# Performance work log

Measured on AMD Instinct MI355X. Metric: run time of the kernel, lower is better.

The kernel has to match this reference:

```python
import jax, jax.numpy as jnp
import numpy as np

K_MASK = -2.3819763e38  # gemma masking constant


def apply_rope(inputs, positions, head_dim):
    # inputs: [B, T, N, H], positions: [B, T]
    half = head_dim // 2
    fraction = 2.0 * jnp.arange(half, dtype=jnp.float32) / head_dim
    timescale = 10000.0 ** fraction                      # [half]
    sinusoid = positions[..., None].astype(jnp.float32) / timescale  # [B, T, half]
    sin = jnp.sin(sinusoid)[:, :, None, :]               # [B, T, 1, half]
    cos = jnp.cos(sinusoid)[:, :, None, :]
    first, second = jnp.split(inputs, 2, axis=-1)
    out = jnp.concatenate([first * cos - second * sin,
                           second * cos + first * sin], axis=-1)
    return out.astype(inputs.dtype)


def setup_inputs() -> dict:
    key = jax.random.key(0)
    k0, k1, k2, k3 = jax.random.split(key, 4)
    B, T, D, N, H = 4, 1024, 2048, 16, 128
    x = jax.random.normal(k0, (B, T, D), dtype=jnp.float32)
    wq = jax.random.normal(k1, (N, D, H), dtype=jnp.float32) * 0.02
    wkv = jax.random.normal(k2, (2, 1, D, H), dtype=jnp.float32) * 0.02  # MQA: 1 kv head
    wo = jax.random.normal(k3, (N, H, D), dtype=jnp.float32) * 0.02
    segment_pos = jnp.broadcast_to(jnp.arange(T, dtype=jnp.int32), (B, T))
    attn_mask = jnp.broadcast_to(jnp.tril(jnp.ones((T, T), dtype=bool)), (B, T, T))
    return {"x": x, "wq": wq, "wkv": wkv, "wo": wo,
            "segment_pos": segment_pos, "attn_mask": attn_mask}


def reference(x, wq, wkv, wo, segment_pos, attn_mask):
    N, _, H = wq.shape
    # projections
    q = jnp.einsum('BTD,NDH->BTNH', x, wq)          # [B,T,N,H]
    kv = jnp.einsum('BSD,CKDH->CBSKH', x, wkv)      # [2,B,S,1,H]
    k, v = kv[0], kv[1]
    # RoPE + scaling
    q = apply_rope(q, segment_pos, H) * (H ** -0.5)
    k = apply_rope(k, segment_pos, H)
    # MQA head repeat: 1 kv head -> N heads
    k = jnp.repeat(k, N, axis=-2)                   # [B,S,N,H]
    v = jnp.repeat(v, N, axis=-2)
    # attention with manual masked softmax
    logits = jnp.einsum('BTNH,BSNH->BTNS', q, k)
    padded = jnp.where(attn_mask[:, :, None, :], logits, K_MASK)
    probs = jax.nn.softmax(padded, axis=-1).astype(k.dtype)
    encoded = jnp.einsum('BTNS,BSNH->BTNH', probs, v)
    return jnp.einsum('BTNH,NHD->BTD', encoded, wo)
```

## Files before the change

### kernel.cpp

```cpp
#include <hip/hip_runtime.h>
#include <cstdint>
#include <cstddef>

typedef unsigned short u16;
typedef __attribute__((ext_vector_type(8))) short bf16x8;
typedef __attribute__((ext_vector_type(4))) float f32x4;
typedef __attribute__((ext_vector_type(16))) float f32x16;
typedef __attribute__((ext_vector_type(4))) uint32_t u32x4;

#define B_ 4
#define T_ 1024
#define D_ 2048
#define N_ 16
#define H_ 128
#define BT_ (B_ * T_)
#define KMASK (-2.3819763e38f)

__device__ __forceinline__ u16 f2bf(float f) {
  uint32_t u = __builtin_bit_cast(uint32_t, f);
  u += 0x7FFFu + ((u >> 16) & 1u);
  return (u16)(u >> 16);
}
__device__ __forceinline__ float bf2f(uint32_t u) {
  return __builtin_bit_cast(float, u << 16);
}

__device__ __forceinline__ float xhalf_max(float x) {
  return fmaxf(x, __shfl_xor(x, 32, 64));
}
__device__ __forceinline__ float xhalf_add(float x) {
  return x + __shfl_xor(x, 32, 64);
}

__device__ __forceinline__ void gload16(const void* g, void* l) {
  __builtin_amdgcn_global_load_lds((const __attribute__((address_space(1))) void*)g,
                                   (__attribute__((address_space(3))) void*)l, 16, 0, 0);
}

__global__ __launch_bounds__(256) void convert_x_kernel(const float* __restrict__ x,
                                                        u16* __restrict__ xb) {
  int i = (blockIdx.x * 256 + threadIdx.x) * 8;
  float4 v0 = *(const float4*)(x + i);
  float4 v1 = *(const float4*)(x + i + 4);
  uint4 o;
  o.x = (uint32_t)f2bf(v0.x) | ((uint32_t)f2bf(v0.y) << 16);
  o.y = (uint32_t)f2bf(v0.z) | ((uint32_t)f2bf(v0.w) << 16);
  o.z = (uint32_t)f2bf(v1.x) | ((uint32_t)f2bf(v1.y) << 16);
  o.w = (uint32_t)f2bf(v1.z) | ((uint32_t)f2bf(v1.w) << 16);
  *(uint4*)(xb + i) = o;
}

__global__ __launch_bounds__(256) void transpose_kernel(const float* __restrict__ src,
                                                        u16* __restrict__ dst, int R, int C) {
  __shared__ float tile[32][33];
  const int z = blockIdx.z;
  const float* s = src + (size_t)z * R * C;
  u16* d = dst + (size_t)z * R * C;
  const int tx = threadIdx.x, ty = threadIdx.y;
  const int r0 = blockIdx.y * 32, c0 = blockIdx.x * 32;
#pragma unroll
  for (int i = 0; i < 4; ++i)
    tile[ty + i * 8][tx] = s[(size_t)(r0 + ty + i * 8) * C + (c0 + tx)];
  __syncthreads();
#pragma unroll
  for (int i = 0; i < 4; ++i)
    d[(size_t)(c0 + ty + i * 8) * R + (r0 + tx)] = f2bf(tile[tx][ty + i * 8]);
}

__global__ __launch_bounds__(256) void rope_table_kernel(float* __restrict__ costab,
                                                         float* __restrict__ sintab) {
  int idx = blockIdx.x * 256 + threadIdx.x;
  int p = idx >> 6, i = idx & 63;
  float ts = powf(10000.0f, (float)i * (1.0f / 64.0f));
  float ang = (float)p / ts;
  costab[idx] = cosf(ang);
  sintab[idx] = sinf(ang);
}

__global__ __launch_bounds__(256) void proj_gemm_kernel(
    const u16* __restrict__ xb, const u16* __restrict__ wqT, const u16* __restrict__ wkvT,
    u16* __restrict__ qraw, u16* __restrict__ kraw, u16* __restrict__ vT) {
  __shared__ alignas(16) u16 a_lds[128 * 64];
  __shared__ alignas(16) u16 b_lds[128 * 64];
  const int bid = blockIdx.x;
  const int newbid = (bid & 7) * 72 + (bid >> 3);
  const int y = newbid >> 5;
  const int m0 = (newbid & 31) * 128;
  const u16* Bt = (y < N_) ? (wqT + (size_t)y * H_ * D_) : (wkvT + (size_t)(y - N_) * H_ * D_);
  const int tid = threadIdx.x;
  const int w = tid >> 6, lane = tid & 63;
  const int g = lane >> 4, li = lane & 15;
  const int mrow = (w >> 1) * 64, wc = (w & 1) * 64;
  f32x4 acc[4][4];
#pragma unroll
  for (int i = 0; i < 4; ++i)
#pragma unroll
    for (int j = 0; j < 4; ++j) acc[i][j] = (f32x4){0.f, 0.f, 0.f, 0.f};

  for (int k0 = 0; k0 < D_; k0 += 64) {
    __syncthreads();
#pragma unroll
    for (int it = 0; it < 4; ++it) {
      int chunk = it * 256 + tid;
      int row = chunk >> 3, cu = chunk & 7;
      gload16(xb + (size_t)(m0 + row) * D_ + k0 + ((cu ^ (row & 7)) << 3), &a_lds[chunk * 8]);
    }
#pragma unroll
    for (int it = 0; it < 4; ++it) {
      int chunk = it * 256 + tid;
      int row = chunk >> 3, cu = chunk & 7;
      gload16(Bt + (size_t)row * D_ + k0 + ((cu ^ (row & 7)) << 3), &b_lds[chunk * 8]);
    }
    __syncthreads();
#pragma unroll
    for (int c2 = 0; c2 < 2; ++c2) {
      bf16x8 af[4], bfr[4];
#pragma unroll
      for (int i = 0; i < 4; ++i) {
        int row = mrow + i * 16 + li;
        af[i] = *(const bf16x8*)((const char*)a_lds +
                                 row * 128 + ((c2 * 64 + g * 16) ^ ((row & 7) << 4)));
      }
#pragma unroll
      for (int j = 0; j < 4; ++j) {
        int row = wc + j * 16 + li;
        bfr[j] = *(const bf16x8*)((const char*)b_lds +
                                  row * 128 + ((c2 * 64 + g * 16) ^ ((row & 7) << 4)));
      }
#pragma unroll
      for (int i = 0; i < 4; ++i)
#pragma unroll
        for (int j = 0; j < 4; ++j)
          acc[i][j] = __builtin_amdgcn_mfma_f32_16x16x32_bf16(af[i], bfr[j], acc[i][j], 0, 0, 0);
    }
  }

  const int b = m0 >> 10;
  if (y == N_ + 1) {
    const int tbase0 = (m0 & 1023) + mrow;
#pragma unroll
    for (int i = 0; i < 4; ++i) {
      int tbase = tbase0 + i * 16 + g * 4;
#pragma unroll
      for (int j = 0; j < 4; ++j) {
        int h = wc + j * 16 + li;
        ushort4 pk;
        pk.x = f2bf(acc[i][j][0]);
        pk.y = f2bf(acc[i][j][1]);
        pk.z = f2bf(acc[i][j][2]);
        pk.w = f2bf(acc[i][j][3]);
        *(ushort4*)(vT + ((size_t)(b * H_ + h)) * T_ + tbase) = pk;
      }
    }
  } else {
    size_t rowbase = (y < N_) ? ((size_t)(b * N_ + y) * T_ + (m0 & 1023)) : (size_t)m0;
    u16* dst0 = (y < N_) ? qraw : kraw;
#pragma unroll
    for (int i = 0; i < 4; ++i)
#pragma unroll
      for (int r = 0; r < 4; ++r) {
        int trow = mrow + i * 16 + g * 4 + r;
        u16* dst = dst0 + (rowbase + trow) * H_;
#pragma unroll
        for (int j = 0; j < 4; ++j) dst[wc + j * 16 + li] = f2bf(acc[i][j][r]);
      }
  }
}

__global__ __launch_bounds__(256) void rope_apply_k_kernel(
    const u16* __restrict__ kraw, const int* __restrict__ segment_pos,
    const float* __restrict__ costab, const float* __restrict__ sintab,
    u16* __restrict__ kb) {
  const int rid = blockIdx.x * 8 + (threadIdx.x >> 5);
  const int j = threadIdx.x & 31;
  const u16* src = kraw + (size_t)rid * H_;
  u16* dst = kb + (size_t)rid * H_;
  int p = segment_pos[rid];
  p = p < 0 ? 0 : (p > 1023 ? 1023 : p);
  uint32_t ua = *(const uint32_t*)(src + 2 * j);
  uint32_t ub = *(const uint32_t*)(src + 64 + 2 * j);
  float2 cv = *(const float2*)(costab + p * 64 + 2 * j);
  float2 sv = *(const float2*)(sintab + p * 64 + 2 * j);
  float f1a = bf2f(ua & 0xffffu), f1b = bf2f(ua >> 16);
  float f2a = bf2f(ub & 0xffffu), f2b = bf2f(ub >> 16);
  *(uint32_t*)(dst + 2 * j) =
      (uint32_t)f2bf(f1a * cv.x - f2a * sv.x) | ((uint32_t)f2bf(f1b * cv.y - f2b * sv.y) << 16);
  *(uint32_t*)(dst + 64 + 2 * j) =
      (uint32_t)f2bf(f2a * cv.x + f1a * sv.x) | ((uint32_t)f2bf(f2b * cv.y + f1b * sv.y) << 16);
}

__global__ __launch_bounds__(128) void attn_kernel(
    const u16* __restrict__ qraw, const u16* __restrict__ kb, const u16* __restrict__ vT,
    const int* __restrict__ segment_pos, const float* __restrict__ costab,
    const float* __restrict__ sintab, u16* __restrict__ enc) {
  __shared__ alignas(16) u16 k_lds[2][64 * 128];
  __shared__ alignas(16) u16 v_lds[128 * 64];
  const int bx = blockIdx.x;
  const int qt = 15 - (bx >> 6);
  const int bn = bx & 63;
  const int b = bn >> 4, n = bn & 15;
  const int tid = threadIdx.x, w = tid >> 6, lane = tid & 63;
  const int l31 = lane & 31, hi = lane >> 5;
  const int t = qt * 64 + w * 32 + l31;

  bf16x8 qf[8];
  {
    const u16* qrow = qraw + ((size_t)(b * N_ + n) * T_ + t) * H_;
#pragma unroll
    for (int kc = 0; kc < 8; ++kc) qf[kc] = *(const bf16x8*)(qrow + kc * 16 + hi * 8);
    int p = segment_pos[b * T_ + t];
    p = p < 0 ? 0 : (p > 1023 ? 1023 : p);
    const float scale = 0.12751743342f;
#pragma unroll
    for (int kc = 0; kc < 4; ++kc) {
      const float* cp = costab + p * 64 + kc * 16 + hi * 8;
      const float* sp = sintab + p * 64 + kc * 16 + hi * 8;
#pragma unroll
      for (int e = 0; e < 8; ++e) {
        float cv = cp[e], sv = sp[e];
        float f1 = bf2f((u16)qf[kc][e]);
        float f2 = bf2f((u16)qf[kc + 4][e]);
        qf[kc][e] = (short)f2bf((f1 * cv - f2 * sv) * scale);
        qf[kc + 4][e] = (short)f2bf((f2 * cv + f1 * sv) * scale);
      }
    }
  }

  f32x16 o[4];
#pragma unroll
  for (int hc = 0; hc < 4; ++hc)
#pragma unroll
    for (int r = 0; r < 16; ++r) o[hc][r] = 0.f;
  float m_ = -3e38f, lsum = 0.f;

  auto stageK = [&](int buf, int s0) {
#pragma unroll
    for (int it = 0; it < 8; ++it) {
      int chunk = it * 128 + tid;
      int row = chunk >> 4, cu = chunk & 15;
      gload16(kb + ((size_t)b * T_ + s0 + row) * H_ + ((cu ^ (row & 15)) << 3),
              &k_lds[buf][chunk * 8]);
    }
  };
  auto stageV = [&](int s0) {
#pragma unroll
    for (int it = 0; it < 8; ++it) {
      int chunk = it * 128 + tid;
      int row = chunk >> 3, cu = chunk & 7;
      gload16(vT + ((size_t)(b * H_ + row)) * T_ + s0 + ((cu ^ (row & 7)) << 3),
              &v_lds[chunk * 8]);
    }
  };

  const int nst = qt + 1;
  stageK(0, 0);
  int cur = 0;
  for (int st = 0; st < nst; ++st) {
    const int s0 = st * 64;
    const bool pre = (st + 1 < nst);
    stageV(s0);
    if (pre) stageK(cur ^ 1, s0 + 64);
    if (pre) asm volatile("s_waitcnt vmcnt(16)" ::: "memory");
    else     asm volatile("s_waitcnt vmcnt(8)" ::: "memory");
    __builtin_amdgcn_sched_barrier(0);
    __builtin_amdgcn_s_barrier();

    f32x16 sacc[2];
#pragma unroll
    for (int sub = 0; sub < 2; ++sub)
#pragma unroll
      for (int r = 0; r < 16; ++r) sacc[sub][r] = 0.f;
    __builtin_amdgcn_s_setprio(1);
#pragma unroll
    for (int kc = 0; kc < 8; ++kc)
#pragma unroll
      for (int sub = 0; sub < 2; ++sub) {
        int srow = sub * 32 + l31;
        bf16x8 kf = *(const bf16x8*)((const char*)&k_lds[cur][0] + srow * 256 +
                                     ((kc * 32 + hi * 16) ^ ((srow & 15) << 4)));
        sacc[sub] = __builtin_amdgcn_mfma_f32_32x32x16_bf16(kf, qf[kc], sacc[sub], 0, 0, 0);
      }
    __builtin_amdgcn_s_setprio(0);

    if (st == qt) {
#pragma unroll
      for (int sub = 0; sub < 2; ++sub)
#pragma unroll
        for (int r = 0; r < 16; ++r) {
          int s = s0 + sub * 32 + (r & 3) + 8 * (r >> 2) + 4 * hi;
          if (s > t) sacc[sub][r] = KMASK;
        }
    }

    float mx = -3e38f;
#pragma unroll
    for (int sub = 0; sub < 2; ++sub)
#pragma unroll
      for (int r = 0; r < 16; ++r) mx = fmaxf(mx, sacc[sub][r]);
    mx = xhalf_max(mx);
    if (__any(mx - m_ > 11.5f)) {
      float mn = fmaxf(m_, mx);
      float alpha = exp2f(m_ - mn);
      m_ = mn;
      lsum *= alpha;
#pragma unroll
      for (int hc = 0; hc < 4; ++hc)
#pragma unroll
        for (int r = 0; r < 16; ++r) o[hc][r] *= alpha;
    }
    float ps = 0.f;
#pragma unroll
    for (int sub = 0; sub < 2; ++sub)
#pragma unroll
      for (int r = 0; r < 16; ++r) {
        float pv = exp2f(sacc[sub][r] - m_);
        sacc[sub][r] = pv;
        ps += pv;
      }
    lsum += xhalf_add(ps);

    if (pre) asm volatile("s_waitcnt vmcnt(8)" ::: "memory");
    else     asm volatile("s_waitcnt vmcnt(0)" ::: "memory");
    __builtin_amdgcn_sched_barrier(0);
    __builtin_amdgcn_s_barrier();

    __builtin_amdgcn_s_setprio(1);
#pragma unroll
    for (int sc = 0; sc < 4; ++sc) {
      const int sub = sc >> 1, rb = (sc & 1) * 8;
      uint32_t a0, a1, b0, b1;
      asm("v_cvt_pk_bf16_f32 %0, %1, %2" : "=v"(a0) : "v"(sacc[sub][rb + 0]), "v"(sacc[sub][rb + 1]));
      asm("v_cvt_pk_bf16_f32 %0, %1, %2" : "=v"(a1) : "v"(sacc[sub][rb + 2]), "v"(sacc[sub][rb + 3]));
      asm("v_cvt_pk_bf16_f32 %0, %1, %2" : "=v"(b0) : "v"(sacc[sub][rb + 4]), "v"(sacc[sub][rb + 5]));
      asm("v_cvt_pk_bf16_f32 %0, %1, %2" : "=v"(b1) : "v"(sacc[sub][rb + 6]), "v"(sacc[sub][rb + 7]));
      uint32_t pa0 = (uint32_t)__shfl_xor((int)a0, 32, 64);
      uint32_t pa1 = (uint32_t)__shfl_xor((int)a1, 32, 64);
      uint32_t pb0 = (uint32_t)__shfl_xor((int)b0, 32, 64);
      uint32_t pb1 = (uint32_t)__shfl_xor((int)b1, 32, 64);
      uint32_t d0 = hi ? pb0 : a0;
      uint32_t d1 = hi ? pb1 : a1;
      uint32_t d2 = hi ? b0 : pa0;
      uint32_t d3 = hi ? b1 : pa1;
      u32x4 pdv = (u32x4){d0, d1, d2, d3};
      bf16x8 pf = __builtin_bit_cast(bf16x8, pdv);
#pragma unroll
      for (int hc = 0; hc < 4; ++hc) {
        int hrow = hc * 32 + l31;
        bf16x8 vf = *(const bf16x8*)((const char*)v_lds + hrow * 128 +
                                     ((sc * 32 + hi * 16) ^ ((hrow & 7) << 4)));
        o[hc] = __builtin_amdgcn_mfma_f32_32x32x16_bf16(vf, pf, o[hc], 0, 0, 0);
      }
    }
    __builtin_amdgcn_s_setprio(0);
    __builtin_amdgcn_s_barrier();
    cur ^= 1;
  }

  float inv = 1.0f / lsum;
  u16* dst = enc + ((size_t)(b * T_ + t)) * (N_ * H_) + n * H_;
#pragma unroll
  for (int hc = 0; hc < 4; ++hc)
#pragma unroll
    for (int rq = 0; rq < 4; ++rq) {
      ushort4 pk;
      pk.x = f2bf(o[hc][rq * 4 + 0] * inv);
      pk.y = f2bf(o[hc][rq * 4 + 1] * inv);
      pk.z = f2bf(o[hc][rq * 4 + 2] * inv);
      pk.w = f2bf(o[hc][rq * 4 + 3] * inv);
      *(ushort4*)(dst + hc * 32 + rq * 8 + hi * 4) = pk;
    }
}

__global__ __launch_bounds__(256) void out_gemm_kernel(const u16* __restrict__ enc,
                                                       const u16* __restrict__ woT,
                                                       float* __restrict__ out) {
  __shared__ alignas(16) u16 a_lds[128 * 64];
  __shared__ alignas(16) u16 b_lds[128 * 64];
  const int bid = blockIdx.x;
  const int newbid = (bid & 7) * 64 + (bid >> 3);
  const int m0 = (newbid & 31) * 128;
  const int n0 = (newbid >> 5) * 128;
  const int tid = threadIdx.x, w = tid >> 6, lane = tid & 63;
  const int g = lane >> 4, li = lane & 15;
  const int mrow = (w >> 1) * 64, wc = (w & 1) * 64;
  f32x4 acc[4][4];
#pragma unroll
  for (int i = 0; i < 4; ++i)
#pragma unroll
    for (int j = 0; j < 4; ++j) acc[i][j] = (f32x4){0.f, 0.f, 0.f, 0.f};

  for (int k0 = 0; k0 < D_; k0 += 64) {
    __syncthreads();
#pragma unroll
    for (int it = 0; it < 4; ++it) {
      int chunk = it * 256 + tid;
      int row = chunk >> 3, cu = chunk & 7;
      gload16(enc + (size_t)(m0 + row) * D_ + k0 + ((cu ^ (row & 7)) << 3), &a_lds[chunk * 8]);
    }
#pragma unroll
    for (int it = 0; it < 4; ++it) {
      int chunk = it * 256 + tid;
      int row = chunk >> 3, cu = chunk & 7;
      gload16(woT + (size_t)(n0 + row) * D_ + k0 + ((cu ^ (row & 7)) << 3), &b_lds[chunk * 8]);
    }
    __syncthreads();
#pragma unroll
    for (int c2 = 0; c2 < 2; ++c2) {
      bf16x8 af[4], bfr[4];
#pragma unroll
      for (int i = 0; i < 4; ++i) {
        int row = mrow + i * 16 + li;
        af[i] = *(const bf16x8*)((const char*)a_lds +
                                 row * 128 + ((c2 * 64 + g * 16) ^ ((row & 7) << 4)));
      }
#pragma unroll
      for (int j = 0; j < 4; ++j) {
        int row = wc + j * 16 + li;
        bfr[j] = *(const bf16x8*)((const char*)b_lds +
                                  row * 128 + ((c2 * 64 + g * 16) ^ ((row & 7) << 4)));
      }
#pragma unroll
      for (int i = 0; i < 4; ++i)
#pragma unroll
        for (int j = 0; j < 4; ++j)
          acc[i][j] = __builtin_amdgcn_mfma_f32_16x16x32_bf16(af[i], bfr[j], acc[i][j], 0, 0, 0);
    }
  }
#pragma unroll
  for (int i = 0; i < 4; ++i)
#pragma unroll
    for (int r = 0; r < 4; ++r) {
      int bt = m0 + mrow + i * 16 + g * 4 + r;
      float* dst = out + (size_t)bt * D_ + n0 + wc;
#pragma unroll
      for (int j = 0; j < 4; ++j) dst[j * 16 + li] = acc[i][j][r];
    }
}

extern "C" void kernel_launch(void* const* d_in, const int* in_sizes, int n_in,
                              void* d_out, int out_size, void* d_ws, size_t ws_size,
                              hipStream_t stream) {
  const float* x = (const float*)d_in[0];
  const float* wq = (const float*)d_in[1];
  const float* wkv = (const float*)d_in[2];
  const float* wo = (const float*)d_in[3];
  const int* segment_pos = (const int*)d_in[4];
  float* out = (float*)d_out;

  char* ws = (char*)d_ws;
  size_t off = 0;
  auto alloc = [&](size_t bytes) -> void* {
    void* p = ws + off;
    off += (bytes + 255) & ~(size_t)255;
    return p;
  };
  u16* xb   = (u16*)alloc((size_t)BT_ * D_ * 2);
  u16* wqT  = (u16*)alloc((size_t)N_ * H_ * D_ * 2);
  u16* wkvT = (u16*)alloc((size_t)2 * H_ * D_ * 2);
  u16* woT  = (u16*)alloc((size_t)D_ * N_ * H_ * 2);
  u16* qraw = (u16*)alloc((size_t)B_ * N_ * T_ * H_ * 2);
  u16* kb   = (u16*)alloc((size_t)B_ * T_ * H_ * 2);
  u16* kraw = (u16*)alloc((size_t)B_ * T_ * H_ * 2);
  u16* vT   = (u16*)alloc((size_t)B_ * H_ * T_ * 2);
  u16* enc  = (u16*)alloc((size_t)BT_ * N_ * H_ * 2);
  float* costab = (float*)alloc(1024 * 64 * 4);
  float* sintab = (float*)alloc(1024 * 64 * 4);

  convert_x_kernel<<<BT_ * D_ / 8 / 256, 256, 0, stream>>>(x, xb);
  dim3 tb(32, 8);
  transpose_kernel<<<dim3(H_ / 32, D_ / 32, N_), tb, 0, stream>>>(wq, wqT, D_, H_);
  transpose_kernel<<<dim3(H_ / 32, D_ / 32, 2), tb, 0, stream>>>(wkv, wkvT, D_, H_);
  transpose_kernel<<<dim3(D_ / 32, D_ / 32, 1), tb, 0, stream>>>(wo, woT, N_ * H_, D_);
  rope_table_kernel<<<256, 256, 0, stream>>>(costab, sintab);
  proj_gemm_kernel<<<576, 256, 0, stream>>>(xb, wqT, wkvT, qraw, kraw, vT);
  rope_apply_k_kernel<<<BT_ / 8, 256, 0, stream>>>(kraw, segment_pos, costab, sintab, kb);
  attn_kernel<<<1024, 128, 0, stream>>>(qraw, kb, vT, segment_pos, costab, sintab, enc);
  out_gemm_kernel<<<512, 256, 0, stream>>>(enc, woT, out);
}
```

Before: 180.1 us.

## Fuse RoPE and query scaling into projection GEMM epilogue via LDS staging

The projection GEMM epilogue now stages its bf16 tile in shared memory, then applies RoPE (and the 1/sqrt(H) scale for queries) before writing Q and K rows with coalesced 32-bit stores. This removes the separate K RoPE kernel, the kraw round trip, and the per-block Q RoPE prologue in the attention kernel. In exchange it adds an extra LDS pass and two barriers to the GEMM epilogue. It also reuses the A/B LDS buffers for staging.

```diff
diff --git a/kernel.cpp b/kernel.cpp
--- a/kernel.cpp
+++ b/kernel.cpp
@@ -79,9 +79,10 @@
 
 __global__ __launch_bounds__(256) void proj_gemm_kernel(
     const u16* __restrict__ xb, const u16* __restrict__ wqT, const u16* __restrict__ wkvT,
-    u16* __restrict__ qraw, u16* __restrict__ kraw, u16* __restrict__ vT) {
-  __shared__ alignas(16) u16 a_lds[128 * 64];
-  __shared__ alignas(16) u16 b_lds[128 * 64];
+    const int* __restrict__ segment_pos, const float* __restrict__ costab,
+    const float* __restrict__ sintab, u16* __restrict__ qb, u16* __restrict__ kbuf,
+    u16* __restrict__ vT) {
+  __shared__ alignas(16) u16 lds[2][128 * 64];
   const int bid = blockIdx.x;
   const int newbid = (bid & 7) * 72 + (bid >> 3);
   const int y = newbid >> 5;
@@ -103,13 +104,13 @@
     for (int it = 0; it < 4; ++it) {
       int chunk = it * 256 + tid;
       int row = chunk >> 3, cu = chunk & 7;
-      gload16(xb + (size_t)(m0 + row) * D_ + k0 + ((cu ^ (row & 7)) << 3), &a_lds[chunk * 8]);
+      gload16(xb + (size_t)(m0 + row) * D_ + k0 + ((cu ^ (row & 7)) << 3), &lds[0][chunk * 8]);
     }
 #pragma unroll
     for (int it = 0; it < 4; ++it) {
       int chunk = it * 256 + tid;
       int row = chunk >> 3, cu = chunk & 7;
-      gload16(Bt + (size_t)row * D_ + k0 + ((cu ^ (row & 7)) << 3), &b_lds[chunk * 8]);
+      gload16(Bt + (size_t)row * D_ + k0 + ((cu ^ (row & 7)) << 3), &lds[1][chunk * 8]);
     }
     __syncthreads();
 #pragma unroll
@@ -118,13 +119,13 @@
 #pragma unroll
       for (int i = 0; i < 4; ++i) {
         int row = mrow + i * 16 + li;
-        af[i] = *(const bf16x8*)((const char*)a_lds +
+        af[i] = *(const bf16x8*)((const char*)&lds[0][0] +
                                  row * 128 + ((c2 * 64 + g * 16) ^ ((row & 7) << 4)));
       }
 #pragma unroll
       for (int j = 0; j < 4; ++j) {
         int row = wc + j * 16 + li;
-        bfr[j] = *(const bf16x8*)((const char*)b_lds +
+        bfr[j] = *(const bf16x8*)((const char*)&lds[1][0] +
                                   row * 128 + ((c2 * 64 + g * 16) ^ ((row & 7) << 4)));
       }
 #pragma unroll
@@ -153,46 +154,49 @@
       }
     }
   } else {
-    size_t rowbase = (y < N_) ? ((size_t)(b * N_ + y) * T_ + (m0 & 1023)) : (size_t)m0;
-    u16* dst0 = (y < N_) ? qraw : kraw;
+    u16* flat = &lds[0][0];
+    __syncthreads();
 #pragma unroll
     for (int i = 0; i < 4; ++i)
 #pragma unroll
       for (int r = 0; r < 4; ++r) {
-        int trow = mrow + i * 16 + g * 4 + r;
-        u16* dst = dst0 + (rowbase + trow) * H_;
-#pragma unroll
-        for (int j = 0; j < 4; ++j) dst[wc + j * 16 + li] = f2bf(acc[i][j][r]);
-      }
+        int row = mrow + i * 16 + g * 4 + r;
+#pragma unroll
+        for (int j = 0; j < 4; ++j) flat[row * 128 + wc + j * 16 + li] = f2bf(acc[i][j][r]);
+      }
+    __syncthreads();
+    const int row = tid >> 1, half = tid & 1;
+    const int bt = m0 + row;
+    int p = segment_pos[bt];
+    p = p < 0 ? 0 : (p > 1023 ? 1023 : p);
+    const float scale = (y < N_) ? 0.12751743342f : 1.0f;
+    u16* dstrow = (y < N_) ? (qb + ((size_t)(b * N_ + y) * T_ + (bt & (T_ - 1))) * H_)
+                           : (kbuf + (size_t)bt * H_);
+    uint32_t* dst32 = (uint32_t*)dstrow;
+    const uint32_t* f32p = (const uint32_t*)flat + row * 64;
+    const float* cp = costab + p * 64 + 32 * half;
+    const float* sp = sintab + p * 64 + 32 * half;
+#pragma unroll
+    for (int c = 0; c < 16; ++c) {
+      uint32_t ua = f32p[16 * half + c];
+      uint32_t ub = f32p[32 + 16 * half + c];
+      float cv0 = cp[2 * c], cv1 = cp[2 * c + 1];
+      float sv0 = sp[2 * c], sv1 = sp[2 * c + 1];
+      float f1a = bf2f(ua & 0xffffu), f1b = bf2f(ua >> 16);
+      float f2a = bf2f(ub & 0xffffu), f2b = bf2f(ub >> 16);
+      uint32_t o1 = (uint32_t)f2bf((f1a * cv0 - f2a * sv0) * scale) |
+                    ((uint32_t)f2bf((f1b * cv1 - f2b * sv1) * scale) << 16);
+      uint32_t o2 = (uint32_t)f2bf((f2a * cv0 + f1a * sv0) * scale) |
+                    ((uint32_t)f2bf((f2b * cv1 + f1b * sv1) * scale) << 16);
+      dst32[16 * half + c] = o1;
+      dst32[32 + 16 * half + c] = o2;
+    }
   }
 }
 
-__global__ __launch_bounds__(256) void rope_apply_k_kernel(
-    const u16* __restrict__ kraw, const int* __restrict__ segment_pos,
-    const float* __restrict__ costab, const float* __restrict__ sintab,
-    u16* __restrict__ kb) {
-  const int rid = blockIdx.x * 8 + (threadIdx.x >> 5);
-  const int j = threadIdx.x & 31;
-  const u16* src = kraw + (size_t)rid * H_;
-  u16* dst = kb + (size_t)rid * H_;
-  int p = segment_pos[rid];
-  p = p < 0 ? 0 : (p > 1023 ? 1023 : p);
-  uint32_t ua = *(const uint32_t*)(src + 2 * j);
-  uint32_t ub = *(const uint32_t*)(src + 64 + 2 * j);
-  float2 cv = *(const float2*)(costab + p * 64 + 2 * j);
-  float2 sv = *(const float2*)(sintab + p * 64 + 2 * j);
-  float f1a = bf2f(ua & 0xffffu), f1b = bf2f(ua >> 16);
-  float f2a = bf2f(ub & 0xffffu), f2b = bf2f(ub >> 16);
-  *(uint32_t*)(dst + 2 * j) =
-      (uint32_t)f2bf(f1a * cv.x - f2a * sv.x) | ((uint32_t)f2bf(f1b * cv.y - f2b * sv.y) << 16);
-  *(uint32_t*)(dst + 64 + 2 * j) =
-      (uint32_t)f2bf(f2a * cv.x + f1a * sv.x) | ((uint32_t)f2bf(f2b * cv.y + f1b * sv.y) << 16);
-}
-
 __global__ __launch_bounds__(128) void attn_kernel(
-    const u16* __restrict__ qraw, const u16* __restrict__ kb, const u16* __restrict__ vT,
-    const int* __restrict__ segment_pos, const float* __restrict__ costab,
-    const float* __restrict__ sintab, u16* __restrict__ enc) {
+    const u16* __restrict__ qb, const u16* __restrict__ kb, const u16* __restrict__ vT,
+    u16* __restrict__ enc) {
   __shared__ alignas(16) u16 k_lds[2][64 * 128];
   __shared__ alignas(16) u16 v_lds[128 * 64];
   const int bx = blockIdx.x;
@@ -205,25 +209,9 @@
 
   bf16x8 qf[8];
   {
-    const u16* qrow = qraw + ((size_t)(b * N_ + n) * T_ + t) * H_;
+    const u16* qrow = qb + ((size_t)(b * N_ + n) * T_ + t) * H_;
 #pragma unroll
     for (int kc = 0; kc < 8; ++kc) qf[kc] = *(const bf16x8*)(qrow + kc * 16 + hi * 8);
-    int p = segment_pos[b * T_ + t];
-    p = p < 0 ? 0 : (p > 1023 ? 1023 : p);
-    const float scale = 0.12751743342f;
-#pragma unroll
-    for (int kc = 0; kc < 4; ++kc) {
-      const float* cp = costab + p * 64 + kc * 16 + hi * 8;
-      const float* sp = sintab + p * 64 + kc * 16 + hi * 8;
-#pragma unroll
-      for (int e = 0; e < 8; ++e) {
-        float cv = cp[e], sv = sp[e];
-        float f1 = bf2f((u16)qf[kc][e]);
-        float f2 = bf2f((u16)qf[kc + 4][e]);
-        qf[kc][e] = (short)f2bf((f1 * cv - f2 * sv) * scale);
-        qf[kc + 4][e] = (short)f2bf((f2 * cv + f1 * sv) * scale);
-      }
-    }
   }
 
   f32x16 o[4];
@@ -458,9 +446,8 @@
   u16* wqT  = (u16*)alloc((size_t)N_ * H_ * D_ * 2);
   u16* wkvT = (u16*)alloc((size_t)2 * H_ * D_ * 2);
   u16* woT  = (u16*)alloc((size_t)D_ * N_ * H_ * 2);
-  u16* qraw = (u16*)alloc((size_t)B_ * N_ * T_ * H_ * 2);
+  u16* qb   = (u16*)alloc((size_t)B_ * N_ * T_ * H_ * 2);
   u16* kb   = (u16*)alloc((size_t)B_ * T_ * H_ * 2);
-  u16* kraw = (u16*)alloc((size_t)B_ * T_ * H_ * 2);
   u16* vT   = (u16*)alloc((size_t)B_ * H_ * T_ * 2);
   u16* enc  = (u16*)alloc((size_t)BT_ * N_ * H_ * 2);
   float* costab = (float*)alloc(1024 * 64 * 4);
@@ -472,8 +459,8 @@
   transpose_kernel<<<dim3(H_ / 32, D_ / 32, 2), tb, 0, stream>>>(wkv, wkvT, D_, H_);
   transpose_kernel<<<dim3(D_ / 32, D_ / 32, 1), tb, 0, stream>>>(wo, woT, N_ * H_, D_);
   rope_table_kernel<<<256, 256, 0, stream>>>(costab, sintab);
-  proj_gemm_kernel<<<576, 256, 0, stream>>>(xb, wqT, wkvT, qraw, kraw, vT);
-  rope_apply_k_kernel<<<BT_ / 8, 256, 0, stream>>>(kraw, segment_pos, costab, sintab, kb);
-  attn_kernel<<<1024, 128, 0, stream>>>(qraw, kb, vT, segment_pos, costab, sintab, enc);
+  proj_gemm_kernel<<<576, 256, 0, stream>>>(xb, wqT, wkvT, segment_pos, costab, sintab,
+                                            qb, kb, vT);
+  attn_kernel<<<1024, 128, 0, stream>>>(qb, kb, vT, enc);
   out_gemm_kernel<<<512, 256, 0, stream>>>(enc, woT, out);
 }
```

Result: slower. 248.5 us (+38.0%).
